# Kernel tuning notes

Hardware: AMD Instinct MI355X
Metric: run time of the kernel (lower is better)

The kernel has to match this reference:

```python
import jax, jax.numpy as jnp
import numpy as np

HIDDEN = 2048
N_HEADS = 16
HEAD_DIM = 128
N_KV_HEADS = 4
MAX_POS = 4096
NEG_INF = -1e9


def _fixed_pos_embedding(features, length):
    # matches generate_fixed_pos_embedding: freqs over arange(0, features, 2)/features
    fraction = jnp.arange(0, features, 2, dtype=jnp.float32) / features
    timescale = 10000.0 ** fraction
    inv_freq = 1.0 / timescale
    sinusoid = jnp.einsum('i,j->ij', jnp.arange(length, dtype=jnp.float32), inv_freq)
    sinusoid = jnp.concatenate([sinusoid, sinusoid], axis=-1)  # [length, features]
    return jnp.sin(sinusoid), jnp.cos(sinusoid)


def setup_inputs() -> dict:
    key = jax.random.key(0)
    k0, k1, k2, k3, k4 = jax.random.split(key, 5)
    B, S = 2, 2048
    hidden_states = jax.random.normal(k0, (B, S, HIDDEN), dtype=jnp.float32)
    # causal additive mask [B,1,S,S]; module forces mask[:, :, :, 0] = 0
    causal = jnp.where(jnp.tril(jnp.ones((S, S), dtype=bool)), 0.0, NEG_INF).astype(jnp.float32)
    causal = causal.at[:, 0].set(0.0)
    attention_mask = jnp.broadcast_to(causal[None, None], (B, 1, S, S))
    std = 0.02
    q_w = jax.random.normal(k1, (N_HEADS * HEAD_DIM, HIDDEN), dtype=jnp.float32) * std
    k_w = jax.random.normal(k2, (N_KV_HEADS * HEAD_DIM, HIDDEN), dtype=jnp.float32) * std
    v_w = jax.random.normal(k3, (N_KV_HEADS * HEAD_DIM, HIDDEN), dtype=jnp.float32) * std
    o_w = jax.random.normal(k4, (HIDDEN, N_HEADS * HEAD_DIM), dtype=jnp.float32) * std
    sin, cos = _fixed_pos_embedding(HEAD_DIM, MAX_POS)
    return {"hidden_states": hidden_states, "attention_mask": attention_mask,
            "q_w": q_w, "k_w": k_w, "v_w": v_w, "o_w": o_w, "sin": sin, "cos": cos}


def _rotate_half(x):
    d = x.shape[-1] // 2
    return jnp.concatenate([-x[..., d:], x[..., :d]], axis=-1)


def reference(hidden_states, attention_mask, q_w, k_w, v_w, o_w, sin, cos):
    B, S, _ = hidden_states.shape
    D = cos.shape[-1]
    H = q_w.shape[0] // D
    KV = k_w.shape[0] // D
    n_rep = H // KV

    # QKV projections (nn.Linear: y = x @ W^T), split into heads: [B,S,h,D]
    q = jnp.einsum('bsh,oh->bso', hidden_states, q_w).reshape(B, S, H, D)
    k = jnp.einsum('bsh,oh->bso', hidden_states, k_w).reshape(B, S, KV, D)
    v = jnp.einsum('bsh,oh->bso', hidden_states, v_w).reshape(B, S, KV, D)

    # rotary embedding (non-decode path: q and k share cos/sin[:S])
    c = cos[:S][None, :, None, :]
    s = sin[:S][None, :, None, :]
    q = q * c + _rotate_half(q) * s
    k = k * c + _rotate_half(k) * s

    # repeat_kv (repeat_interleave along head dim) for GQA
    k = jnp.repeat(k, n_rep, axis=2)  # [B,S,H,D]
    v = jnp.repeat(v, n_rep, axis=2)

    # NOTE: no 1/sqrt(D) scaling -- module uses softmax_scale=1.0
    scores = jnp.einsum('bqhd,bkhd->bhqk', q, k) + attention_mask
    weights = jax.nn.softmax(scores.astype(jnp.float32), axis=-1).astype(q.dtype)
    attn = jnp.einsum('bhqk,bkhd->bqhd', weights, v).reshape(B, S, H * D)
    return jnp.einsum('bso,ho->bsh', attn, o_w)
```

## Files before the change

### kernel.cpp

```cpp
#include <hip/hip_runtime.h>

typedef __bf16 bf16x8 __attribute__((ext_vector_type(8)));
typedef float f32x4 __attribute__((ext_vector_type(4)));

#define LOG2E 1.44269504088896340736f

#define GLDS16(g, l) __builtin_amdgcn_global_load_lds(                         \
    (const __attribute__((address_space(1))) unsigned int*)(g),                \
    (__attribute__((address_space(3))) unsigned int*)(l), 16, 0, 0)


__global__ __launch_bounds__(256) void split_matrix(
    const float* __restrict__ src, __bf16* __restrict__ dh, __bf16* __restrict__ dl)
{
    const size_t t = (size_t)(blockIdx.x * 256 + threadIdx.x) * 8;
    float4 a = *(const float4*)(src + t);
    float4 b = *(const float4*)(src + t + 4);
    float f[8] = {a.x, a.y, a.z, a.w, b.x, b.y, b.z, b.w};
    bf16x8 h, l;
#pragma unroll
    for (int i = 0; i < 8; ++i) {
        __bf16 hh = (__bf16)f[i];
        h[i] = hh; l[i] = (__bf16)(f[i] - (float)hh);
    }
    const int r  = (int)(t >> 11);
    const int sw = (r ^ (r >> 2)) & 3;
    const size_t d = (t & ~(size_t)31) + ((size_t)((((int)(t >> 3) & 3) ^ sw)) << 3);
    *(bf16x8*)(dh + d) = h;
    *(bf16x8*)(dl + d) = l;
}

template<int BN, int NLOAD>
__global__ __launch_bounds__(512, 2) void gemm_planes8(
    const __bf16* __restrict__ Ah, const __bf16* __restrict__ Al,
    const __bf16* __restrict__ Bh, const __bf16* __restrict__ Bl,
    float* __restrict__ C, int ldc)
{
    constexpr int WN = BN / 4;
    constexpr int NF = WN / 16;

    __shared__ __bf16 sAh[2][256 * 32];
    __shared__ __bf16 sAl[2][256 * 32];
    __shared__ __bf16 sBh[2][BN * 32];
    __shared__ __bf16 sBl[2][BN * 32];

    const int tid  = threadIdx.x;
    const int lane = tid & 63;
    const int wave = tid >> 6;
    const int wm   = (wave & 1) * 128;
    const int wn   = (wave >> 1) * WN;

    const int idg = blockIdx.y * 16 + blockIdx.x;
    const int swb = (idg & 7) * 32 + (idg >> 3);
    const int m0  = (swb >> 4) * 256;
    const int n0  = (swb & 15) * BN;

    const int fr  = lane & 15;
    const int g   = lane >> 4;
    const int dr  = g * 4;
    const int sxr = (fr ^ (fr >> 2)) & 3;
    const int pA  = (g ^ sxr) << 3;

    const int srow = tid >> 2;
    const int spb  = (tid & 3) << 3;
    const __bf16* gAh0 = Ah + (size_t)(m0 + srow) * 2048 + spb;
    const __bf16* gAh1 = gAh0 + (size_t)128 * 2048;
    const __bf16* gAl0 = Al + (size_t)(m0 + srow) * 2048 + spb;
    const __bf16* gAl1 = gAl0 + (size_t)128 * 2048;
    const __bf16* gBh0 = Bh + (size_t)(n0 + srow) * 2048 + spb;
    const __bf16* gBl0 = Bl + (size_t)(n0 + srow) * 2048 + spb;
    const __bf16* gX5  = Bl;
    const __bf16* gBl6 = Bl;
    if constexpr (BN == 192) {
        gX5 = (tid < 256)
            ? Bh + (size_t)(n0 + 128 + srow) * 2048 + spb
            : Bl + (size_t)(n0 + ((tid - 256) >> 2)) * 2048 + (((tid - 256) & 3) << 3);
        gBl6 = Bl + (size_t)(n0 + 64 + srow) * 2048 + spb;
    }

#define STAGE8(bb)                                                             \
    do {                                                                       \
        GLDS16(gAh0, &sAh[bb][tid * 8]);                                       \
        GLDS16(gAh1, &sAh[bb][4096 + tid * 8]);                                \
        GLDS16(gAl0, &sAl[bb][tid * 8]);                                       \
        GLDS16(gAl1, &sAl[bb][4096 + tid * 8]);                                \
        GLDS16(gBh0, &sBh[bb][tid * 8]);                                       \
        if constexpr (BN == 192) {                                             \
            if (tid < 256) { GLDS16(gX5, &sBh[bb][4096 + tid * 8]); }          \
            else           { GLDS16(gX5, &sBl[bb][(tid - 256) * 8]); }         \
            GLDS16(gBl6, &sBl[bb][2048 + tid * 8]);                            \
        } else {                                                               \
            GLDS16(gBl0, &sBl[bb][tid * 8]);                                   \
        }                                                                      \
    } while (0)

#define ADV8()                                                                 \
    do {                                                                       \
        gAh0 += 32; gAh1 += 32; gAl0 += 32; gAl1 += 32;                        \
        gBh0 += 32; gBl0 += 32;                                                \
        if constexpr (BN == 192) { gX5 += 32; gBl6 += 32; }                    \
    } while (0)

    f32x4 acc[8][NF];
#pragma unroll
    for (int mf = 0; mf < 8; ++mf)
#pragma unroll
        for (int nf = 0; nf < NF; ++nf)
            acc[mf][nf] = (f32x4){0.f, 0.f, 0.f, 0.f};

    STAGE8(0);
    ADV8();

    for (int t = 0; t < 64; ++t) {
        const int buf = t & 1;
        if (t < 63) {
            STAGE8(buf ^ 1);
            ADV8();
            __builtin_amdgcn_sched_barrier(0);
            if constexpr (NLOAD == 7) asm volatile("s_waitcnt vmcnt(7)" ::: "memory");
            else                      asm volatile("s_waitcnt vmcnt(6)" ::: "memory");
        } else {
            __builtin_amdgcn_sched_barrier(0);
            asm volatile("s_waitcnt vmcnt(0)" ::: "memory");
        }
        __builtin_amdgcn_sched_barrier(0);
        __builtin_amdgcn_s_barrier();
        __builtin_amdgcn_sched_barrier(0);

        bf16x8 bh[NF], bl[NF];
#pragma unroll
        for (int p = 0; p < 4; ++p) {
            if (p == 0) {
#pragma unroll
                for (int nf = 0; nf < NF; ++nf) {
                    bh[nf] = *(const bf16x8*)&sBh[buf][(wn + nf * 16 + fr) * 32 + pA];
                    bl[nf] = *(const bf16x8*)&sBl[buf][(wn + nf * 16 + fr) * 32 + pA];
                }
            }
            bf16x8 a0h = *(const bf16x8*)&sAh[buf][(wm + p * 32 + fr) * 32 + pA];
            bf16x8 a0l = *(const bf16x8*)&sAl[buf][(wm + p * 32 + fr) * 32 + pA];
            bf16x8 a1h = *(const bf16x8*)&sAh[buf][(wm + p * 32 + 16 + fr) * 32 + pA];
            bf16x8 a1l = *(const bf16x8*)&sAl[buf][(wm + p * 32 + 16 + fr) * 32 + pA];
            __builtin_amdgcn_sched_barrier(0);
            __builtin_amdgcn_s_barrier();
            __builtin_amdgcn_sched_barrier(0);
            __builtin_amdgcn_s_setprio(1);
#pragma unroll
            for (int nf = 0; nf < NF; ++nf) {
                acc[2 * p][nf] = __builtin_amdgcn_mfma_f32_16x16x32_bf16(a0h, bh[nf], acc[2 * p][nf], 0, 0, 0);
                acc[2 * p][nf] = __builtin_amdgcn_mfma_f32_16x16x32_bf16(a0l, bh[nf], acc[2 * p][nf], 0, 0, 0);
                acc[2 * p][nf] = __builtin_amdgcn_mfma_f32_16x16x32_bf16(a0h, bl[nf], acc[2 * p][nf], 0, 0, 0);
                acc[2 * p + 1][nf] = __builtin_amdgcn_mfma_f32_16x16x32_bf16(a1h, bh[nf], acc[2 * p + 1][nf], 0, 0, 0);
                acc[2 * p + 1][nf] = __builtin_amdgcn_mfma_f32_16x16x32_bf16(a1l, bh[nf], acc[2 * p + 1][nf], 0, 0, 0);
                acc[2 * p + 1][nf] = __builtin_amdgcn_mfma_f32_16x16x32_bf16(a1h, bl[nf], acc[2 * p + 1][nf], 0, 0, 0);
            }
            __builtin_amdgcn_s_setprio(0);
        }
    }

#pragma unroll
    for (int mf = 0; mf < 8; ++mf)
#pragma unroll
        for (int nf = 0; nf < NF; ++nf)
#pragma unroll
            for (int rr = 0; rr < 4; ++rr) {
                const int row = m0 + wm + mf * 16 + dr + rr;
                const int col = n0 + wn + nf * 16 + fr;
                C[(size_t)row * ldc + col] = acc[mf][nf][rr];
            }
#undef STAGE8
#undef ADV8
}

__global__ __launch_bounds__(256) void rope_q(
    float* __restrict__ qkv,
    const float* __restrict__ sinp, const float* __restrict__ cosp)
{
    int t = blockIdx.x * 256 + threadIdx.x;
    int row = t >> 10;
    int rem = t & 1023;
    int col = (rem >> 6) * 128 + (rem & 63);
    int s = row & 2047;
    int d = col & 127;

    float* p = qkv + (size_t)row * 3072 + col;
    float x0  = p[0];
    float x1  = p[64];
    float c0  = cosp[s * 128 + d];
    float c1  = cosp[s * 128 + d + 64];
    float sn0 = sinp[s * 128 + d];
    float sn1 = sinp[s * 128 + d + 64];
    p[0]  = x0 * c0 - x1 * sn0;
    p[64] = x1 * c1 + x0 * sn1;
}

__global__ __launch_bounds__(256) void prep_kv(
    const float* __restrict__ qkv,
    const float* __restrict__ sinp, const float* __restrict__ cosp,
    __bf16* __restrict__ ksp, __bf16* __restrict__ vtsp)
{
    __shared__ float vs[32][132];

    const int tid = threadIdx.x;
    const int kb  = blockIdx.x;
    const int kvh = blockIdx.y;
    const int b   = blockIdx.z;

    {
        const int key = tid >> 1;
        const int dh  = (tid & 1) * 32;
        const int pos = kb * 128 + key;
        const int ksw = key & 7;
        const float* src = qkv + (size_t)(b * 2048 + pos) * 3072 + 2048 + kvh * 128;
        __bf16* dst = ksp + ((size_t)((b * 4 + kvh) * 2048) + pos) * 256;
        const float* cp = cosp + pos * 128;
        const float* sp = sinp + pos * 128;
#pragma unroll
        for (int g = 0; g < 4; ++g) {
            int d0 = dh + g * 8;
            float4 x0a = *(const float4*)(src + d0);
            float4 x0b = *(const float4*)(src + d0 + 4);
            float4 x1a = *(const float4*)(src + d0 + 64);
            float4 x1b = *(const float4*)(src + d0 + 68);
            float4 c0a = *(const float4*)(cp + d0);
            float4 c0b = *(const float4*)(cp + d0 + 4);
            float4 c1a = *(const float4*)(cp + d0 + 64);
            float4 c1b = *(const float4*)(cp + d0 + 68);
            float4 s0a = *(const float4*)(sp + d0);
            float4 s0b = *(const float4*)(sp + d0 + 4);
            float4 s1a = *(const float4*)(sp + d0 + 64);
            float4 s1b = *(const float4*)(sp + d0 + 68);
            float x0[8] = {x0a.x,x0a.y,x0a.z,x0a.w,x0b.x,x0b.y,x0b.z,x0b.w};
            float x1[8] = {x1a.x,x1a.y,x1a.z,x1a.w,x1b.x,x1b.y,x1b.z,x1b.w};
            float c0[8] = {c0a.x,c0a.y,c0a.z,c0a.w,c0b.x,c0b.y,c0b.z,c0b.w};
            float c1[8] = {c1a.x,c1a.y,c1a.z,c1a.w,c1b.x,c1b.y,c1b.z,c1b.w};
            float s0[8] = {s0a.x,s0a.y,s0a.z,s0a.w,s0b.x,s0b.y,s0b.z,s0b.w};
            float s1[8] = {s1a.x,s1a.y,s1a.z,s1a.w,s1b.x,s1b.y,s1b.z,s1b.w};
            bf16x8 h0, l0, h1, l1;
#pragma unroll
            for (int i = 0; i < 8; ++i) {
                float y0 = x0[i] * c0[i] - x1[i] * s0[i];
                float y1 = x1[i] * c1[i] + x0[i] * s1[i];
                __bf16 hh0 = (__bf16)y0;
                __bf16 hh1 = (__bf16)y1;
                h0[i] = hh0; l0[i] = (__bf16)(y0 - (float)hh0);
                h1[i] = hh1; l1[i] = (__bf16)(y1 - (float)hh1);
            }
            const int bb = d0 >> 3;
            *(bf16x8*)(dst + ((bb        ^ ksw) << 3)) = h0;
            *(bf16x8*)(dst + (((bb + 8)  ^ ksw) << 3)) = h1;
            *(bf16x8*)(dst + (((bb + 16) ^ ksw) << 3)) = l0;
            *(bf16x8*)(dst + (((bb + 24) ^ ksw) << 3)) = l1;
        }
    }

    for (int st = 0; st < 4; ++st) {
        __syncthreads();
        {
            const int key = tid >> 3;
            const int dc  = (tid & 7) * 16;
            const float* vsrc = qkv + (size_t)(b * 2048 + kb * 128 + st * 32 + key) * 3072
                                + 2560 + kvh * 128 + dc;
            float4 v0 = *(const float4*)(vsrc);
            float4 v1 = *(const float4*)(vsrc + 4);
            float4 v2 = *(const float4*)(vsrc + 8);
            float4 v3 = *(const float4*)(vsrc + 12);
            *(float4*)&vs[key][dc]      = v0;
            *(float4*)&vs[key][dc + 4]  = v1;
            *(float4*)&vs[key][dc + 8]  = v2;
            *(float4*)&vs[key][dc + 12] = v3;
        }
        __syncthreads();
        {
            const int plane = tid >> 7;
            const int d     = tid & 127;
            bf16x8 ob[4];
#pragma unroll
            for (int k = 0; k < 32; ++k) {
                float x = vs[k][d];
                __bf16 hh = (__bf16)x;
                ob[k >> 3][k & 7] = plane ? (__bf16)(x - (float)hh) : hh;
            }
            const int rV  = plane * 128 + d;
            const int vsw = (d >> 1) & 3;
            __bf16* dst = vtsp + ((size_t)((b * 4 + kvh) * 64 + kb * 4 + st)) * 8192
                               + (size_t)rV * 32;
            *(bf16x8*)(dst + ((0 ^ vsw) << 3)) = ob[0];
            *(bf16x8*)(dst + ((1 ^ vsw) << 3)) = ob[1];
            *(bf16x8*)(dst + ((2 ^ vsw) << 3)) = ob[2];
            *(bf16x8*)(dst + ((3 ^ vsw) << 3)) = ob[3];
        }
    }
}

__global__ __launch_bounds__(256, 2) void flash_attn(
    const float* __restrict__ qkv,
    const __bf16* __restrict__ ksp,
    const __bf16* __restrict__ vtsp,
    __bf16* __restrict__ attnh, __bf16* __restrict__ attnl)
{
    __shared__ __bf16 Ks[2][32 * 256];
    __shared__ __bf16 Vt[2][256 * 32];
    __shared__ unsigned int Psf[4][2][512];

    const int tid  = threadIdx.x;
    const int lane = tid & 63;
    const int wave = tid >> 6;
    const int id   = blockIdx.x;
    const int pair = id & 7;
    const int kvh  = pair & 3;
    const int b    = pair >> 2;
    const int u    = id >> 3;
    const int qb   = (u >> 5) ? (u & 31) : 63 - (u & 31);
    const int h    = kvh * 4 + wave;

    const int fr  = lane & 15;
    const int g   = lane >> 4;
    const int fc  = g * 8;
    const int dr  = g * 4;
    const int frs = fr & 7;

    bf16x8 aqh[2][4], aql[2][4];
    for (int rs = 0; rs < 2; ++rs) {
        const size_t qrow = (size_t)(b * 2048 + qb * 32 + rs * 16 + fr) * 3072 + h * 128;
        for (int ks = 0; ks < 4; ++ks) {
            float4 qv[2];
            qv[0] = *(const float4*)(qkv + qrow + ks * 32 + fc);
            qv[1] = *(const float4*)(qkv + qrow + ks * 32 + fc + 4);
            const float* qf = (const float*)qv;
            bf16x8 h8, l8;
#pragma unroll
            for (int i = 0; i < 8; ++i) {
                float x = qf[i];
                __bf16 hh = (__bf16)x;
                h8[i] = hh; l8[i] = (__bf16)(x - (float)hh);
            }
            aqh[rs][ks] = h8; aql[rs][ks] = l8;
        }
    }
    asm volatile("s_waitcnt vmcnt(0)" ::: "memory");
    __builtin_amdgcn_sched_barrier(0);

    bf16x8 ones;
#pragma unroll
    for (int i = 0; i < 8; ++i) ones[i] = (__bf16)1.0f;

    f32x4 o[2][8];
    for (int rs = 0; rs < 2; ++rs)
        for (int dg = 0; dg < 8; ++dg) o[rs][dg] = (f32x4){0.f, 0.f, 0.f, 0.f};
    f32x4 ls[2] = {(f32x4){0.f,0.f,0.f,0.f}, (f32x4){0.f,0.f,0.f,0.f}};

    const int ntiles = qb + 1;
    const __bf16* kg0 = ksp + (size_t)(b * 4 + kvh) * 2048 * 256 + wave * 2048 + lane * 8;
    const __bf16* vg0 = vtsp + (size_t)(b * 4 + kvh) * 64 * 8192 + wave * 2048 + lane * 8;

    {
        __bf16* kl = &Ks[0][wave * 2048];
        __bf16* vl = &Vt[0][wave * 2048];
        GLDS16(kg0,        kl);       GLDS16(kg0 + 512,  kl + 512);
        GLDS16(kg0 + 1024, kl + 1024);GLDS16(kg0 + 1536, kl + 1536);
        GLDS16(vg0,        vl);       GLDS16(vg0 + 512,  vl + 512);
        GLDS16(vg0 + 1024, vl + 1024);GLDS16(vg0 + 1536, vl + 1536);
    }

    for (int kt = 0; kt < ntiles; ++kt) {
        if (kt + 1 < ntiles) {
            const __bf16* kg = kg0 + (size_t)(kt + 1) * 8192;
            const __bf16* vg = vg0 + (size_t)(kt + 1) * 8192;
            __bf16* kl = &Ks[(kt + 1) & 1][wave * 2048];
            __bf16* vl = &Vt[(kt + 1) & 1][wave * 2048];
            GLDS16(kg,        kl);       GLDS16(kg + 512,  kl + 512);
            GLDS16(kg + 1024, kl + 1024);GLDS16(kg + 1536, kl + 1536);
            GLDS16(vg,        vl);       GLDS16(vg + 512,  vl + 512);
            GLDS16(vg + 1024, vl + 1024);GLDS16(vg + 1536, vl + 1536);
            asm volatile("s_waitcnt vmcnt(8)" ::: "memory");
        } else {
            asm volatile("s_waitcnt vmcnt(0)" ::: "memory");
        }
        __builtin_amdgcn_sched_barrier(0);
        __builtin_amdgcn_s_barrier();
        __builtin_amdgcn_sched_barrier(0);

        const int buf = kt & 1;
        const int k0 = kt * 32;

        f32x4 s[2][2];
        s[0][0] = s[0][1] = s[1][0] = s[1][1] = (f32x4){0.f, 0.f, 0.f, 0.f};
        __builtin_amdgcn_s_setprio(1);
#pragma unroll
        for (int ks = 0; ks < 4; ++ks) {
            const int bh = ks * 4 + g;
            bf16x8 b0h = *(const bf16x8*)&Ks[buf][fr * 256        + ((bh        ^ frs) << 3)];
            bf16x8 b0l = *(const bf16x8*)&Ks[buf][fr * 256        + (((bh + 16) ^ frs) << 3)];
            bf16x8 b1h = *(const bf16x8*)&Ks[buf][(16 + fr) * 256 + ((bh        ^ frs) << 3)];
            bf16x8 b1l = *(const bf16x8*)&Ks[buf][(16 + fr) * 256 + (((bh + 16) ^ frs) << 3)];
#pragma unroll
            for (int rs = 0; rs < 2; ++rs) {
                s[rs][0] = __builtin_amdgcn_mfma_f32_16x16x32_bf16(aqh[rs][ks], b0h, s[rs][0], 0, 0, 0);
                s[rs][0] = __builtin_amdgcn_mfma_f32_16x16x32_bf16(aql[rs][ks], b0h, s[rs][0], 0, 0, 0);
                s[rs][0] = __builtin_amdgcn_mfma_f32_16x16x32_bf16(aqh[rs][ks], b0l, s[rs][0], 0, 0, 0);
                s[rs][1] = __builtin_amdgcn_mfma_f32_16x16x32_bf16(aqh[rs][ks], b1h, s[rs][1], 0, 0, 0);
                s[rs][1] = __builtin_amdgcn_mfma_f32_16x16x32_bf16(aql[rs][ks], b1h, s[rs][1], 0, 0, 0);
                s[rs][1] = __builtin_amdgcn_mfma_f32_16x16x32_bf16(aqh[rs][ks], b1l, s[rs][1], 0, 0, 0);
            }
        }
        __builtin_amdgcn_s_setprio(0);

        const bool diag = (kt == ntiles - 1);
#pragma unroll
        for (int rs = 0; rs < 2; ++rs) {
            f32x4 s0 = s[rs][0], s1 = s[rs][1];
            if (diag) {
#pragma unroll
                for (int r = 0; r < 4; ++r) {
                    const int qg = qb * 32 + rs * 16 + dr + r;
                    if (k0 + fr > qg)      s0[r] = -1e30f;
                    if (k0 + 16 + fr > qg) s1[r] = -1e30f;
                }
            }
            uint4 w0, w1;
#pragma unroll
            for (int r = 0; r < 4; ++r) {
                float x0 = exp2f(s0[r] * LOG2E);
                float x1 = exp2f(s1[r] * LOG2E);
                __bf16 h0 = (__bf16)x0;
                __bf16 h1 = (__bf16)x1;
                unsigned u0 = ((unsigned)__builtin_bit_cast(unsigned short, h0) << 16)
                            |  (unsigned)__builtin_bit_cast(unsigned short, (__bf16)(x0 - (float)h0));
                unsigned u1 = ((unsigned)__builtin_bit_cast(unsigned short, h1) << 16)
                            |  (unsigned)__builtin_bit_cast(unsigned short, (__bf16)(x1 - (float)h1));
                ((unsigned*)&w0)[r] = u0;
                ((unsigned*)&w1)[r] = u1;
            }
            unsigned int* pw = &Psf[wave][rs][0];
            const int sb = (fr * 4 + g) ^ (((fr >> 3) & 1) << 2);
            *(uint4*)(pw + sb * 4)        = w0;
            *(uint4*)(pw + (sb + 64) * 4) = w1;
        }
        asm volatile("s_waitcnt lgkmcnt(0)" ::: "memory");
        __builtin_amdgcn_sched_barrier(0);

        bf16x8 ph[2], pl[2];
#pragma unroll
        for (int rs = 0; rs < 2; ++rs) {
#pragma unroll
            for (int j = 0; j < 8; ++j) {
                const int col = fc + j;
                const int sR  = (col * 4 + (fr >> 2)) ^ ((g & 1) << 2);
                const unsigned v = Psf[wave][rs][sR * 4 + (fr & 3)];
                ph[rs][j] = __builtin_bit_cast(__bf16, (unsigned short)(v >> 16));
                pl[rs][j] = __builtin_bit_cast(__bf16, (unsigned short)(v & 0xffffu));
            }
        }

        __builtin_amdgcn_s_setprio(1);
        ls[0] = __builtin_amdgcn_mfma_f32_16x16x32_bf16(ph[0], ones, ls[0], 0, 0, 0);
        ls[0] = __builtin_amdgcn_mfma_f32_16x16x32_bf16(pl[0], ones, ls[0], 0, 0, 0);
        ls[1] = __builtin_amdgcn_mfma_f32_16x16x32_bf16(ph[1], ones, ls[1], 0, 0, 0);
        ls[1] = __builtin_amdgcn_mfma_f32_16x16x32_bf16(pl[1], ones, ls[1], 0, 0, 0);
#pragma unroll
        for (int dg = 0; dg < 8; ++dg) {
            const int d0 = dg * 16 + fr;
            const int sw = (g ^ ((d0 >> 1) & 3)) << 3;
            bf16x8 bvh = *(const bf16x8*)&Vt[buf][d0 * 32 + sw];
            bf16x8 bvl = *(const bf16x8*)&Vt[buf][(d0 + 128) * 32 + sw];
#pragma unroll
            for (int rs = 0; rs < 2; ++rs) {
                o[rs][dg] = __builtin_amdgcn_mfma_f32_16x16x32_bf16(ph[rs], bvh, o[rs][dg], 0, 0, 0);
                o[rs][dg] = __builtin_amdgcn_mfma_f32_16x16x32_bf16(pl[rs], bvh, o[rs][dg], 0, 0, 0);
                o[rs][dg] = __builtin_amdgcn_mfma_f32_16x16x32_bf16(ph[rs], bvl, o[rs][dg], 0, 0, 0);
            }
        }
        __builtin_amdgcn_s_setprio(0);

        __builtin_amdgcn_s_barrier();
    }

    for (int rs = 0; rs < 2; ++rs) {
        const size_t orow = (size_t)(b * 2048 + qb * 32 + rs * 16);
        for (int dg = 0; dg < 8; ++dg)
            for (int r = 0; r < 4; ++r) {
                float val = o[rs][dg][r] / ls[rs][r];
                const int rl  = dr + r;
                const int swz = (rl ^ (rl >> 2)) & 3;
                const int col = h * 128 + dg * 16 + fr;
                const size_t idx = (size_t)(orow + rl) * 2048 + (col & ~31)
                                 + ((((col >> 3) & 3) ^ swz) << 3) + (col & 7);
                __bf16 hh = (__bf16)val;
                attnh[idx] = hh;
                attnl[idx] = (__bf16)(val - (float)hh);
            }
    }
}

extern "C" void kernel_launch(void* const* d_in, const int* in_sizes, int n_in,
                              void* d_out, int out_size, void* d_ws, size_t ws_size,
                              hipStream_t stream)
{
    const float* hs   = (const float*)d_in[0];
    const float* qw   = (const float*)d_in[2];
    const float* kw   = (const float*)d_in[3];
    const float* vw   = (const float*)d_in[4];
    const float* ow   = (const float*)d_in[5];
    const float* sinp = (const float*)d_in[6];
    const float* cosp = (const float*)d_in[7];
    float* outp = (float*)d_out;

    char* w = (char*)d_ws;
    float*  qkv  = (float*)w;   w += (size_t)4096 * 3072 * 4;
    __bf16* ksp  = (__bf16*)w;  w += (size_t)8 * 2048 * 256 * 2;
    __bf16* vtsp = (__bf16*)w;  w += (size_t)8 * 64 * 8192 * 2;
    __bf16* wqh  = (__bf16*)w;  w += (size_t)3072 * 2048 * 2;
    __bf16* wql  = (__bf16*)w;  w += (size_t)3072 * 2048 * 2;
    __bf16* owh  = (__bf16*)w;  w += (size_t)2048 * 2048 * 2;
    __bf16* owl  = (__bf16*)w;  w += (size_t)2048 * 2048 * 2;
    __bf16* hsh  = (__bf16*)w;  w += (size_t)4096 * 2048 * 2;
    __bf16* hsl  = (__bf16*)w;  w += (size_t)4096 * 2048 * 2;
    __bf16* attnh = hsh;
    __bf16* attnl = hsl;

    split_matrix<<<4096, 256, 0, stream>>>(hs, hsh, hsl);
    split_matrix<<<2048, 256, 0, stream>>>(qw, wqh, wql);
    split_matrix<<<512,  256, 0, stream>>>(kw, wqh + (size_t)2048 * 2048,
                                               wql + (size_t)2048 * 2048);
    split_matrix<<<512,  256, 0, stream>>>(vw, wqh + (size_t)2560 * 2048,
                                               wql + (size_t)2560 * 2048);
    split_matrix<<<2048, 256, 0, stream>>>(ow, owh, owl);

    gemm_planes8<192, 7><<<dim3(16, 16), 512, 0, stream>>>(hsh, hsl, wqh, wql, qkv, 3072);
    rope_q<<<16384, 256, 0, stream>>>(qkv, sinp, cosp);
    prep_kv<<<dim3(16, 4, 2), 256, 0, stream>>>(qkv, sinp, cosp, ksp, vtsp);
    flash_attn<<<512, 256, 0, stream>>>(qkv, ksp, vtsp, attnh, attnl);
    gemm_planes8<128, 6><<<dim3(16, 16), 512, 0, stream>>>(attnh, attnl, owh, owl, outp, 2048);
}
```

Before: 587.3 us.

## Merge split and rope/prep launches; split flash-attn query rows across 8 waves

The five split_matrix launches become one megasplit kernel that picks its source by block index. rope_q and prep_kv are merged into one launch, which cuts launch overhead. Flash attention now runs 512 threads per block, with each wave handling one head and one 16-row query slice instead of two, and each wave loading half as many K/V chunks. This halves per-wave register use and raises the number of waves per block to increase occupancy, at the cost of more waves sharing the block barrier. The merged rope/prep kernel drops the launch ordering that separated the two stages, so prep_kv blocks may read K/V from the QKV buffer at the same time as rope blocks run.

```diff
diff --git a/kernel.cpp b/kernel.cpp
--- a/kernel.cpp
+++ b/kernel.cpp
@@ -10,10 +10,27 @@
     (__attribute__((address_space(3))) unsigned int*)(l), 16, 0, 0)
 
 
-__global__ __launch_bounds__(256) void split_matrix(
-    const float* __restrict__ src, __bf16* __restrict__ dh, __bf16* __restrict__ dl)
+__global__ __launch_bounds__(256) void megasplit(
+    const float* __restrict__ hs, const float* __restrict__ qw,
+    const float* __restrict__ kw, const float* __restrict__ vw,
+    const float* __restrict__ ow,
+    __bf16* __restrict__ hsh, __bf16* __restrict__ hsl,
+    __bf16* __restrict__ wqh, __bf16* __restrict__ wql,
+    __bf16* __restrict__ owh, __bf16* __restrict__ owl)
 {
-    const size_t t = (size_t)(blockIdx.x * 256 + threadIdx.x) * 8;
+    int bid = blockIdx.x;
+    const float* src; __bf16* dh; __bf16* dl;
+    if (bid < 4096)      { src = hs; dh = hsh; dl = hsl; }
+    else if (bid < 6144) { bid -= 4096; src = qw; dh = wqh; dl = wql; }
+    else if (bid < 6656) { bid -= 6144; src = kw;
+                           dh = wqh + (size_t)2048 * 2048;
+                           dl = wql + (size_t)2048 * 2048; }
+    else if (bid < 7168) { bid -= 6656; src = vw;
+                           dh = wqh + (size_t)2560 * 2048;
+                           dl = wql + (size_t)2560 * 2048; }
+    else                 { bid -= 7168; src = ow; dh = owh; dl = owl; }
+
+    const size_t t = (size_t)(bid * 256 + threadIdx.x) * 8;
     float4 a = *(const float4*)(src + t);
     float4 b = *(const float4*)(src + t + 4);
     float f[8] = {a.x, a.y, a.z, a.w, b.x, b.y, b.z, b.w};
@@ -172,39 +189,38 @@
 #undef ADV8
 }
 
-__global__ __launch_bounds__(256) void rope_q(
+__global__ __launch_bounds__(256) void rope_prep(
     float* __restrict__ qkv,
-    const float* __restrict__ sinp, const float* __restrict__ cosp)
-{
-    int t = blockIdx.x * 256 + threadIdx.x;
-    int row = t >> 10;
-    int rem = t & 1023;
-    int col = (rem >> 6) * 128 + (rem & 63);
-    int s = row & 2047;
-    int d = col & 127;
-
-    float* p = qkv + (size_t)row * 3072 + col;
-    float x0  = p[0];
-    float x1  = p[64];
-    float c0  = cosp[s * 128 + d];
-    float c1  = cosp[s * 128 + d + 64];
-    float sn0 = sinp[s * 128 + d];
-    float sn1 = sinp[s * 128 + d + 64];
-    p[0]  = x0 * c0 - x1 * sn0;
-    p[64] = x1 * c1 + x0 * sn1;
-}
-
-__global__ __launch_bounds__(256) void prep_kv(
-    const float* __restrict__ qkv,
     const float* __restrict__ sinp, const float* __restrict__ cosp,
     __bf16* __restrict__ ksp, __bf16* __restrict__ vtsp)
 {
     __shared__ float vs[32][132];
-
     const int tid = threadIdx.x;
-    const int kb  = blockIdx.x;
-    const int kvh = blockIdx.y;
-    const int b   = blockIdx.z;
+
+    if (blockIdx.x < 16384) {
+        int t = blockIdx.x * 256 + tid;
+        int row = t >> 10;
+        int rem = t & 1023;
+        int col = (rem >> 6) * 128 + (rem & 63);
+        int s = row & 2047;
+        int d = col & 127;
+
+        float* p = qkv + (size_t)row * 3072 + col;
+        float x0  = p[0];
+        float x1  = p[64];
+        float c0  = cosp[s * 128 + d];
+        float c1  = cosp[s * 128 + d + 64];
+        float sn0 = sinp[s * 128 + d];
+        float sn1 = sinp[s * 128 + d + 64];
+        p[0]  = x0 * c0 - x1 * sn0;
+        p[64] = x1 * c1 + x0 * sn1;
+        return;
+    }
+
+    const int pidx = blockIdx.x - 16384;
+    const int kb  = pidx & 15;
+    const int kvh = (pidx >> 4) & 3;
+    const int b   = pidx >> 6;
 
     {
         const int key = tid >> 1;
@@ -293,7 +309,7 @@
     }
 }
 
-__global__ __launch_bounds__(256, 2) void flash_attn(
+__global__ __launch_bounds__(512, 4) void flash_attn(
     const float* __restrict__ qkv,
     const __bf16* __restrict__ ksp,
     const __bf16* __restrict__ vtsp,
@@ -306,13 +322,15 @@
     const int tid  = threadIdx.x;
     const int lane = tid & 63;
     const int wave = tid >> 6;
+    const int hw   = wave & 3;
+    const int rs   = wave >> 2;
     const int id   = blockIdx.x;
     const int pair = id & 7;
     const int kvh  = pair & 3;
     const int b    = pair >> 2;
     const int u    = id >> 3;
     const int qb   = (u >> 5) ? (u & 31) : 63 - (u & 31);
-    const int h    = kvh * 4 + wave;
+    const int h    = kvh * 4 + hw;
 
     const int fr  = lane & 15;
     const int g   = lane >> 4;
@@ -320,9 +338,10 @@
     const int dr  = g * 4;
     const int frs = fr & 7;
 
-    bf16x8 aqh[2][4], aql[2][4];
-    for (int rs = 0; rs < 2; ++rs) {
+    bf16x8 aqh[4], aql[4];
+    {
         const size_t qrow = (size_t)(b * 2048 + qb * 32 + rs * 16 + fr) * 3072 + h * 128;
+#pragma unroll
         for (int ks = 0; ks < 4; ++ks) {
             float4 qv[2];
             qv[0] = *(const float4*)(qkv + qrow + ks * 32 + fc);
@@ -335,7 +354,7 @@
                 __bf16 hh = (__bf16)x;
                 h8[i] = hh; l8[i] = (__bf16)(x - (float)hh);
             }
-            aqh[rs][ks] = h8; aql[rs][ks] = l8;
+            aqh[ks] = h8; aql[ks] = l8;
         }
     }
     asm volatile("s_waitcnt vmcnt(0)" ::: "memory");
@@ -345,35 +364,31 @@
 #pragma unroll
     for (int i = 0; i < 8; ++i) ones[i] = (__bf16)1.0f;
 
-    f32x4 o[2][8];
-    for (int rs = 0; rs < 2; ++rs)
-        for (int dg = 0; dg < 8; ++dg) o[rs][dg] = (f32x4){0.f, 0.f, 0.f, 0.f};
-    f32x4 ls[2] = {(f32x4){0.f,0.f,0.f,0.f}, (f32x4){0.f,0.f,0.f,0.f}};
+    f32x4 o[8];
+#pragma unroll
+    for (int dg = 0; dg < 8; ++dg) o[dg] = (f32x4){0.f, 0.f, 0.f, 0.f};
+    f32x4 ls = (f32x4){0.f, 0.f, 0.f, 0.f};
 
     const int ntiles = qb + 1;
-    const __bf16* kg0 = ksp + (size_t)(b * 4 + kvh) * 2048 * 256 + wave * 2048 + lane * 8;
-    const __bf16* vg0 = vtsp + (size_t)(b * 4 + kvh) * 64 * 8192 + wave * 2048 + lane * 8;
+    const __bf16* kg0 = ksp + (size_t)(b * 4 + kvh) * 2048 * 256 + wave * 1024 + lane * 8;
+    const __bf16* vg0 = vtsp + (size_t)(b * 4 + kvh) * 64 * 8192 + wave * 1024 + lane * 8;
 
     {
-        __bf16* kl = &Ks[0][wave * 2048];
-        __bf16* vl = &Vt[0][wave * 2048];
-        GLDS16(kg0,        kl);       GLDS16(kg0 + 512,  kl + 512);
-        GLDS16(kg0 + 1024, kl + 1024);GLDS16(kg0 + 1536, kl + 1536);
-        GLDS16(vg0,        vl);       GLDS16(vg0 + 512,  vl + 512);
-        GLDS16(vg0 + 1024, vl + 1024);GLDS16(vg0 + 1536, vl + 1536);
+        __bf16* kl = &Ks[0][wave * 1024];
+        __bf16* vl = &Vt[0][wave * 1024];
+        GLDS16(kg0, kl); GLDS16(kg0 + 512, kl + 512);
+        GLDS16(vg0, vl); GLDS16(vg0 + 512, vl + 512);
     }
 
     for (int kt = 0; kt < ntiles; ++kt) {
         if (kt + 1 < ntiles) {
             const __bf16* kg = kg0 + (size_t)(kt + 1) * 8192;
             const __bf16* vg = vg0 + (size_t)(kt + 1) * 8192;
-            __bf16* kl = &Ks[(kt + 1) & 1][wave * 2048];
-            __bf16* vl = &Vt[(kt + 1) & 1][wave * 2048];
-            GLDS16(kg,        kl);       GLDS16(kg + 512,  kl + 512);
-            GLDS16(kg + 1024, kl + 1024);GLDS16(kg + 1536, kl + 1536);
-            GLDS16(vg,        vl);       GLDS16(vg + 512,  vl + 512);
-            GLDS16(vg + 1024, vl + 1024);GLDS16(vg + 1536, vl + 1536);
-            asm volatile("s_waitcnt vmcnt(8)" ::: "memory");
+            __bf16* kl = &Ks[(kt + 1) & 1][wave * 1024];
+            __bf16* vl = &Vt[(kt + 1) & 1][wave * 1024];
+            GLDS16(kg, kl); GLDS16(kg + 512, kl + 512);
+            GLDS16(vg, vl); GLDS16(vg + 512, vl + 512);
+            asm volatile("s_waitcnt vmcnt(4)" ::: "memory");
         } else {
             asm volatile("s_waitcnt vmcnt(0)" ::: "memory");
         }
@@ -384,8 +399,8 @@
         const int buf = kt & 1;
         const int k0 = kt * 32;
 
-        f32x4 s[2][2];
-        s[0][0] = s[0][1] = s[1][0] = s[1][1] = (f32x4){0.f, 0.f, 0.f, 0.f};
+        f32x4 s0v = (f32x4){0.f, 0.f, 0.f, 0.f};
+        f32x4 s1v = (f32x4){0.f, 0.f, 0.f, 0.f};
         __builtin_amdgcn_s_setprio(1);
 #pragma unroll
         for (int ks = 0; ks < 4; ++ks) {
@@ -394,35 +409,29 @@
             bf16x8 b0l = *(const bf16x8*)&Ks[buf][fr * 256        + (((bh + 16) ^ frs) << 3)];
             bf16x8 b1h = *(const bf16x8*)&Ks[buf][(16 + fr) * 256 + ((bh        ^ frs) << 3)];
             bf16x8 b1l = *(const bf16x8*)&Ks[buf][(16 + fr) * 256 + (((bh + 16) ^ frs) << 3)];
-#pragma unroll
-            for (int rs = 0; rs < 2; ++rs) {
-                s[rs][0] = __builtin_amdgcn_mfma_f32_16x16x32_bf16(aqh[rs][ks], b0h, s[rs][0], 0, 0, 0);
-                s[rs][0] = __builtin_amdgcn_mfma_f32_16x16x32_bf16(aql[rs][ks], b0h, s[rs][0], 0, 0, 0);
-                s[rs][0] = __builtin_amdgcn_mfma_f32_16x16x32_bf16(aqh[rs][ks], b0l, s[rs][0], 0, 0, 0);
-                s[rs][1] = __builtin_amdgcn_mfma_f32_16x16x32_bf16(aqh[rs][ks], b1h, s[rs][1], 0, 0, 0);
-                s[rs][1] = __builtin_amdgcn_mfma_f32_16x16x32_bf16(aql[rs][ks], b1h, s[rs][1], 0, 0, 0);
-                s[rs][1] = __builtin_amdgcn_mfma_f32_16x16x32_bf16(aqh[rs][ks], b1l, s[rs][1], 0, 0, 0);
-            }
+            s0v = __builtin_amdgcn_mfma_f32_16x16x32_bf16(aqh[ks], b0h, s0v, 0, 0, 0);
+            s0v = __builtin_amdgcn_mfma_f32_16x16x32_bf16(aql[ks], b0h, s0v, 0, 0, 0);
+            s0v = __builtin_amdgcn_mfma_f32_16x16x32_bf16(aqh[ks], b0l, s0v, 0, 0, 0);
+            s1v = __builtin_amdgcn_mfma_f32_16x16x32_bf16(aqh[ks], b1h, s1v, 0, 0, 0);
+            s1v = __builtin_amdgcn_mfma_f32_16x16x32_bf16(aql[ks], b1h, s1v, 0, 0, 0);
+            s1v = __builtin_amdgcn_mfma_f32_16x16x32_bf16(aqh[ks], b1l, s1v, 0, 0, 0);
         }
         __builtin_amdgcn_s_setprio(0);
 
-        const bool diag = (kt == ntiles - 1);
-#pragma unroll
-        for (int rs = 0; rs < 2; ++rs) {
-            f32x4 s0 = s[rs][0], s1 = s[rs][1];
-            if (diag) {
-#pragma unroll
-                for (int r = 0; r < 4; ++r) {
-                    const int qg = qb * 32 + rs * 16 + dr + r;
-                    if (k0 + fr > qg)      s0[r] = -1e30f;
-                    if (k0 + 16 + fr > qg) s1[r] = -1e30f;
-                }
-            }
+        if (kt == ntiles - 1) {
+#pragma unroll
+            for (int r = 0; r < 4; ++r) {
+                const int qg = qb * 32 + rs * 16 + dr + r;
+                if (k0 + fr > qg)      s0v[r] = -1e30f;
+                if (k0 + 16 + fr > qg) s1v[r] = -1e30f;
+            }
+        }
+        {
             uint4 w0, w1;
 #pragma unroll
             for (int r = 0; r < 4; ++r) {
-                float x0 = exp2f(s0[r] * LOG2E);
-                float x1 = exp2f(s1[r] * LOG2E);
+                float x0 = exp2f(s0v[r] * LOG2E);
+                float x1 = exp2f(s1v[r] * LOG2E);
                 __bf16 h0 = (__bf16)x0;
                 __bf16 h1 = (__bf16)x1;
                 unsigned u0 = ((unsigned)__builtin_bit_cast(unsigned short, h0) << 16)
@@ -432,7 +441,7 @@
                 ((unsigned*)&w0)[r] = u0;
                 ((unsigned*)&w1)[r] = u1;
             }
-            unsigned int* pw = &Psf[wave][rs][0];
+            unsigned int* pw = &Psf[hw][rs][0];
             const int sb = (fr * 4 + g) ^ (((fr >> 3) & 1) << 2);
             *(uint4*)(pw + sb * 4)        = w0;
             *(uint4*)(pw + (sb + 64) * 4) = w1;
@@ -440,47 +449,41 @@
         asm volatile("s_waitcnt lgkmcnt(0)" ::: "memory");
         __builtin_amdgcn_sched_barrier(0);
 
-        bf16x8 ph[2], pl[2];
-#pragma unroll
-        for (int rs = 0; rs < 2; ++rs) {
-#pragma unroll
-            for (int j = 0; j < 8; ++j) {
-                const int col = fc + j;
-                const int sR  = (col * 4 + (fr >> 2)) ^ ((g & 1) << 2);
-                const unsigned v = Psf[wave][rs][sR * 4 + (fr & 3)];
-                ph[rs][j] = __builtin_bit_cast(__bf16, (unsigned short)(v >> 16));
-                pl[rs][j] = __builtin_bit_cast(__bf16, (unsigned short)(v & 0xffffu));
-            }
+        bf16x8 ph, pl;
+#pragma unroll
+        for (int j = 0; j < 8; ++j) {
+            const int col = fc + j;
+            const int sR  = (col * 4 + (fr >> 2)) ^ ((g & 1) << 2);
+            const unsigned v = Psf[hw][rs][sR * 4 + (fr & 3)];
+            ph[j] = __builtin_bit_cast(__bf16, (unsigned short)(v >> 16));
+            pl[j] = __builtin_bit_cast(__bf16, (unsigned short)(v & 0xffffu));
         }
 
         __builtin_amdgcn_s_setprio(1);
-        ls[0] = __builtin_amdgcn_mfma_f32_16x16x32_bf16(ph[0], ones, ls[0], 0, 0, 0);
-        ls[0] = __builtin_amdgcn_mfma_f32_16x16x32_bf16(pl[0], ones, ls[0], 0, 0, 0);
-        ls[1] = __builtin_amdgcn_mfma_f32_16x16x32_bf16(ph[1], ones, ls[1], 0, 0, 0);
-        ls[1] = __builtin_amdgcn_mfma_f32_16x16x32_bf16(pl[1], ones, ls[1], 0, 0, 0);
+        ls = __builtin_amdgcn_mfma_f32_16x16x32_bf16(ph, ones, ls, 0, 0, 0);
+        ls = __builtin_amdgcn_mfma_f32_16x16x32_bf16(pl, ones, ls, 0, 0, 0);
 #pragma unroll
         for (int dg = 0; dg < 8; ++dg) {
             const int d0 = dg * 16 + fr;
             const int sw = (g ^ ((d0 >> 1) & 3)) << 3;
             bf16x8 bvh = *(const bf16x8*)&Vt[buf][d0 * 32 + sw];
             bf16x8 bvl = *(const bf16x8*)&Vt[buf][(d0 + 128) * 32 + sw];
-#pragma unroll
-            for (int rs = 0; rs < 2; ++rs) {
-                o[rs][dg] = __builtin_amdgcn_mfma_f32_16x16x32_bf16(ph[rs], bvh, o[rs][dg], 0, 0, 0);
-                o[rs][dg] = __builtin_amdgcn_mfma_f32_16x16x32_bf16(pl[rs], bvh, o[rs][dg], 0, 0, 0);
-                o[rs][dg] = __builtin_amdgcn_mfma_f32_16x16x32_bf16(ph[rs], bvl, o[rs][dg], 0, 0, 0);
-            }
+            o[dg] = __builtin_amdgcn_mfma_f32_16x16x32_bf16(ph, bvh, o[dg], 0, 0, 0);
+            o[dg] = __builtin_amdgcn_mfma_f32_16x16x32_bf16(pl, bvh, o[dg], 0, 0, 0);
+            o[dg] = __builtin_amdgcn_mfma_f32_16x16x32_bf16(ph, bvl, o[dg], 0, 0, 0);
         }
         __builtin_amdgcn_s_setprio(0);
 
         __builtin_amdgcn_s_barrier();
     }
 
-    for (int rs = 0; rs < 2; ++rs) {
+    {
         const size_t orow = (size_t)(b * 2048 + qb * 32 + rs * 16);
+#pragma unroll
         for (int dg = 0; dg < 8; ++dg)
+#pragma unroll
             for (int r = 0; r < 4; ++r) {
-                float val = o[rs][dg][r] / ls[rs][r];
+                float val = o[dg][r] / ls[r];
                 const int rl  = dr + r;
                 const int swz = (rl ^ (rl >> 2)) & 3;
                 const int col = h * 128 + dg * 16 + fr;
@@ -519,17 +522,10 @@
     __bf16* attnh = hsh;
     __bf16* attnl = hsl;
 
-    split_matrix<<<4096, 256, 0, stream>>>(hs, hsh, hsl);
-    split_matrix<<<2048, 256, 0, stream>>>(qw, wqh, wql);
-    split_matrix<<<512,  256, 0, stream>>>(kw, wqh + (size_t)2048 * 2048,
-                                               wql + (size_t)2048 * 2048);
-    split_matrix<<<512,  256, 0, stream>>>(vw, wqh + (size_t)2560 * 2048,
-                                               wql + (size_t)2560 * 2048);
-    split_matrix<<<2048, 256, 0, stream>>>(ow, owh, owl);
-
+    megasplit<<<9216, 256, 0, stream>>>(hs, qw, kw, vw, ow,
+                                        hsh, hsl, wqh, wql, owh, owl);
     gemm_planes8<192, 7><<<dim3(16, 16), 512, 0, stream>>>(hsh, hsl, wqh, wql, qkv, 3072);
-    rope_q<<<16384, 256, 0, stream>>>(qkv, sinp, cosp);
-    prep_kv<<<dim3(16, 4, 2), 256, 0, stream>>>(qkv, sinp, cosp, ksp, vtsp);
-    flash_attn<<<512, 256, 0, stream>>>(qkv, ksp, vtsp, attnh, attnl);
+    rope_prep<<<16512, 256, 0, stream>>>(qkv, sinp, cosp, ksp, vtsp);
+    flash_attn<<<512, 512, 0, stream>>>(qkv, ksp, vtsp, attnh, attnl);
     gemm_planes8<128, 6><<<dim3(16, 16), 512, 0, stream>>>(attnh, attnl, owh, owl, outp, 2048);
 }
```

New measurement: 580.8 us. Within noise of the previous version (-1.1%).
